# Optimization experiments

Hardware: AMD Instinct MI355X
Metric: run time of the kernel (lower is better)

## Reference

```python
import jax, jax.numpy as jnp
import numpy as np

K = 20  # neighbors, from init kwarg k

def _knn_idx(x, k):
    # x: [B, C, N]; returns indices of k nearest neighbors [B, N, k]
    xx = jnp.sum(x * x, axis=1)                      # [B, N]
    inner = jnp.einsum('bcn,bcm->bnm', x, x)         # [B, N, N]
    neg_dist = 2.0 * inner - xx[:, :, None] - xx[:, None, :]
    return jax.lax.top_k(neg_dist, k)[1]


def _graph_feature(x, k):
    # x: [B, C, N] -> [B, N, k, 2C] = concat(neighbor - center, center)
    idx = _knn_idx(jax.lax.stop_gradient(x), k)
    xt = jnp.swapaxes(x, 1, 2)                       # [B, N, C]
    nb = jax.vmap(lambda pts, i: pts[i])(xt, idx)    # [B, N, k, C]
    ctr = jnp.broadcast_to(xt[:, :, None, :], nb.shape)
    return jnp.concatenate([nb - ctr, ctr], axis=-1)


def _edge_conv(x, layers, k):
    # x: [B, C, N]; layers: list of (w [Co,Ci], scale [Co], bias [Co])
    g = _graph_feature(x, k)                         # [B, N, k, 2C]
    for w, s, b in layers:
        g = jax.nn.leaky_relu(jnp.einsum('bnkc,oc->bnko', g, w) * s + b, 0.2)
    return jnp.swapaxes(jnp.max(g, axis=2), 1, 2)    # [B, Co, N]


def setup_inputs() -> dict:
    key = jax.random.key(0)
    ks = jax.random.split(key, 20)
    B, N = 2, 8192
    emb = 1024
    def w(k_, shape):
        fan_in = shape[1]
        return jax.random.normal(k_, shape, jnp.float32) * (1.0 / np.sqrt(fan_in))
    def sc(k_, c):
        return jax.random.uniform(k_, (c,), jnp.float32, 0.5, 1.5)
    def bi(k_, c):
        return jax.random.normal(k_, (c,), jnp.float32) * 0.1
    inp = {
        'points': jax.random.normal(ks[0], (B, N, 3), jnp.float32),
        'w1a': w(ks[1], (64, 12)),  's1a': sc(ks[2], 64),  'b1a': bi(ks[3], 64),
        'w1b': w(ks[4], (64, 64)),  's1b': sc(ks[5], 64),  'b1b': bi(ks[6], 64),
        'w2a': w(ks[7], (64, 128)), 's2a': sc(ks[8], 64),  'b2a': bi(ks[9], 64),
        'w2b': w(ks[10], (64, 64)), 's2b': sc(ks[11], 64), 'b2b': bi(ks[12], 64),
        'w3a': w(ks[13], (64, 128)),'s3a': sc(ks[14], 64), 'b3a': bi(ks[15], 64),
        'wg':  w(ks[16], (emb, 192)),'sg': sc(ks[17], emb),'bg': bi(ks[18], emb),
    }
    return inp


def reference(points, w1a, s1a, b1a, w1b, s1b, b1b,
              w2a, s2a, b2a, w2b, s2b, b2b,
              w3a, s3a, b3a, wg, sg, bg):
    B, N, _ = points.shape
    xyz = jnp.swapaxes(points, 1, 2)                 # [B, 3, N]
    x = jnp.concatenate([xyz, xyz], axis=1)          # [B, 6, N] (features == xyz when C==3)
    x1 = _edge_conv(x,  [(w1a, s1a, b1a), (w1b, s1b, b1b)], K)
    x2 = _edge_conv(x1, [(w2a, s2a, b2a), (w2b, s2b, b2b)], K)
    x3 = _edge_conv(x2, [(w3a, s3a, b3a)], K)
    cat = jnp.concatenate([x1, x2, x3], axis=1)      # [B, 192, N]
    h = jax.nn.leaky_relu(
        jnp.einsum('bcn,oc->bon', cat, wg) * sg[None, :, None] + bg[None, :, None], 0.2)
    g = jnp.max(h, axis=-1, keepdims=True)           # [B, emb, 1]
    x_max = jnp.broadcast_to(g, (B, h.shape[1], N))  # [B, emb, N]
    return x_max
```

## Files before the change

kernel.cpp:

```cpp
#include <hip/hip_runtime.h>
#include <hip/hip_bf16.h>

#define NPTS 8192
#define KNN  20
#define KC   4

__device__ __forceinline__ unsigned fkey(float f) {
  unsigned u = __float_as_uint(f);
  return (u & 0x80000000u) ? ~u : (u | 0x80000000u);
}
__device__ __forceinline__ float funkey(unsigned k) {
  return (k & 0x80000000u) ? __uint_as_float(k & 0x7fffffffu) : __uint_as_float(~k);
}
__device__ __forceinline__ float lrelu(float x) { return x >= 0.f ? x : 0.2f * x; }

__global__ __launch_bounds__(256) void prep_kernel(
    const float* __restrict__ w1a, const float* __restrict__ w1b,
    const float* __restrict__ w2a, const float* __restrict__ w2b,
    const float* __restrict__ w3a, const float* __restrict__ wg,
    float* __restrict__ wp1A, float* __restrict__ wp1B,
    float* __restrict__ wp2A, float* __restrict__ wp2B,
    float* __restrict__ wp3A, float* __restrict__ wgT)
{
  const int t0 = blockIdx.x * blockDim.x + threadIdx.x;
  const int NT = gridDim.x * blockDim.x;
  for (int f = t0; f < 512; f += NT) {
    int i = f & 3, o = (f >> 2) & 63, c4 = f >> 8, c = c4 * 4 + i;
    float v = 0.f;
    if (c < 3)      v = w1a[o*12 + c]     + w1a[o*12 + c + 3];
    else if (c < 6) v = w1a[o*12 + c + 3] + w1a[o*12 + c + 6];
    wp1A[f] = v;
  }
  for (int f = t0; f < 4096; f += NT) {
    int i = f & 3, o = (f >> 2) & 63, c4 = f >> 8, c = c4 * 4 + i;
    wp1B[f] = w1b[o*64 + c];
    wp2B[f] = w2b[o*64 + c];
  }
  for (int f = t0; f < 8192; f += NT) {
    int i = f & 3, o = (f >> 2) & 63, c4 = f >> 8, c = c4 * 4 + i;
    wp2A[f] = w2a[o*128 + c];
    wp3A[f] = w3a[o*128 + c];
  }
  for (int f = t0; f < 192 * 1024; f += NT) {
    int c = f >> 10, o = f & 1023;
    wgT[f] = wg[o*192 + c];
  }
}

__global__ __launch_bounds__(256) void xx_points(const float* __restrict__ pts,
                                                 float* __restrict__ xx)
{
  int t = blockIdx.x * 256 + threadIdx.x;
  if (t < 2 * NPTS) {
    const float* p = pts + (size_t)t * 3;
    xx[t] = p[0]*p[0] + p[1]*p[1] + p[2]*p[2];
  }
}

__device__ __forceinline__ void bitonic64_desc_f(float& v, int lane) {
  #pragma unroll
  for (int k = 2; k <= 64; k <<= 1) {
    #pragma unroll
    for (int j = k >> 1; j >= 1; j >>= 1) {
      float o = __shfl_xor(v, j);
      bool take_max = (((lane & k) == 0) == ((lane & j) == 0));
      v = take_max ? fmaxf(v, o) : fminf(v, o);
    }
  }
}

__device__ __forceinline__ void bitonic64_desc_u64(unsigned long long& v, int lane) {
  #pragma unroll
  for (int k = 2; k <= 64; k <<= 1) {
    #pragma unroll
    for (int j = k >> 1; j >= 1; j >>= 1) {
      unsigned long long o = __shfl_xor(v, j);
      bool take_max = (((lane & k) == 0) == ((lane & j) == 0));
      unsigned long long hi = v > o ? v : o;
      unsigned long long lo = v > o ? o : v;
      v = take_max ? hi : lo;
    }
  }
}

__device__ void sel20_half(float* __restrict__ sdh, int half, int lane,
                           float* __restrict__ hv, int* __restrict__ hj,
                           float* __restrict__ cv, int* __restrict__ cj)
{
  float m = -INFINITY;
  const float4* rp = (const float4*)(sdh + lane * 64);
  #pragma unroll
  for (int t = 0; t < 16; ++t) {
    float4 x = rp[(t + lane) & 15];
    m = fmaxf(m, fmaxf(fmaxf(x.x, x.y), fmaxf(x.z, x.w)));
  }
  bitonic64_desc_f(m, lane);
  float That = __shfl(m, 19);

  int base = 0;
  for (int i = 0; i < 64; ++i) {
    float v = sdh[i * 64 + lane];
    bool p = (v >= That);
    unsigned long long mk = __ballot(p);
    if (p) {
      int pos = base + (int)__popcll(mk & ((1ull << lane) - 1ull));
      if (pos < 64) { cv[pos] = v; cj[pos] = i * 64 + lane; }
    }
    base += (int)__popcll(mk);
  }

  if (base <= 64) {
    unsigned long long key = 0ull;
    if (lane < base)
      key = (((unsigned long long)fkey(cv[lane])) << 32) | (unsigned)(~cj[lane]);
    bitonic64_desc_u64(key, lane);
    if (lane < KNN) {
      hv[lane] = funkey((unsigned)(key >> 32));
      hj[lane] = (half << 12) + (int)((~(unsigned)key) & 4095u);
    }
  } else {
    for (int kk = 0; kk < KNN; ++kk) {
      float bv = -INFINITY; int bj = 4096;
      for (int i = 0; i < 64; ++i) {
        float v = sdh[i * 64 + lane];
        if (v > bv) { bv = v; bj = i * 64 + lane; }
      }
      #pragma unroll
      for (int mm = 32; mm >= 1; mm >>= 1) {
        float ov = __shfl_xor(bv, mm); int oj = __shfl_xor(bj, mm);
        if (ov > bv || (ov == bv && oj < bj)) { bv = ov; bj = oj; }
      }
      if (lane == 0) { hv[kk] = bv; hj[kk] = (half << 12) + bj; }
      sdh[bj] = -INFINITY;
    }
  }
}

__device__ __forceinline__ void merge_halves(const float* __restrict__ hv,
                                             const int* __restrict__ hj,
                                             int lane, int* __restrict__ orow)
{
  unsigned long long key = 0ull;
  if (lane < 2 * KNN)
    key = (((unsigned long long)fkey(hv[lane])) << 32) | (unsigned)(~hj[lane]);
  bitonic64_desc_u64(key, lane);
  if (lane < KNN) orow[lane] = (int)((~(unsigned)key) & (NPTS - 1));
}

__global__ __launch_bounds__(512, 4) void knn3_kernel(
    const float* __restrict__ pts, const float* __restrict__ xx,
    int* __restrict__ idxout)
{
  __shared__ __align__(16) float sd[4][4096];
  __shared__ float s_ctr[4][4];
  __shared__ float s_hv[4][2 * KNN];
  __shared__ int   s_hj[4][2 * KNN];
  __shared__ float s_cv[4][64];
  __shared__ int   s_cj[4][64];
  const int tid = threadIdx.x;
  const int b   = blockIdx.x / (NPTS / 4);
  const int r0  = (blockIdx.x % (NPTS / 4)) * 4;
  const size_t rowbase = (size_t)b * NPTS;

  for (int i = tid; i < 12; i += 512)
    s_ctr[i / 3][i % 3] = pts[(rowbase + r0 + i / 3) * 3 + i % 3];
  __syncthreads();

  const float xr0 = xx[rowbase + r0 + 0], xr1 = xx[rowbase + r0 + 1];
  const float xr2 = xx[rowbase + r0 + 2], xr3 = xx[rowbase + r0 + 3];
  const float c00 = s_ctr[0][0], c01 = s_ctr[0][1], c02 = s_ctr[0][2];
  const float c10 = s_ctr[1][0], c11 = s_ctr[1][1], c12 = s_ctr[1][2];
  const float c20 = s_ctr[2][0], c21 = s_ctr[2][1], c22 = s_ctr[2][2];
  const float c30 = s_ctr[3][0], c31 = s_ctr[3][1], c32 = s_ctr[3][2];
  const int wid = tid >> 6, lane = tid & 63;

  #pragma unroll 1
  for (int h = 0; h < 2; ++h) {
    for (int jl = tid; jl < 4096; jl += 512) {
      const int jg = (h << 12) + jl;
      const float* fj = pts + (rowbase + jg) * 3;
      const float f0 = fj[0], f1 = fj[1], f2 = fj[2];
      const float xj = xx[rowbase + jg];
      sd[0][jl] = 2.f*(f0*c00 + f1*c01 + f2*c02) - xr0 - xj;
      sd[1][jl] = 2.f*(f0*c10 + f1*c11 + f2*c12) - xr1 - xj;
      sd[2][jl] = 2.f*(f0*c20 + f1*c21 + f2*c22) - xr2 - xj;
      sd[3][jl] = 2.f*(f0*c30 + f1*c31 + f2*c32) - xr3 - xj;
    }
    __syncthreads();
    if (wid < 4)
      sel20_half(sd[wid], h, lane, &s_hv[wid][h * KNN], &s_hj[wid][h * KNN],
                 s_cv[wid], s_cj[wid]);
    __syncthreads();
  }
  if (wid < 4)
    merge_halves(s_hv[wid], s_hj[wid], lane, idxout + (rowbase + r0 + wid) * KNN);
}

#define ACC4(A, C) \
  A.x += v0.x*C.x + v1.x*C.y + v2.x*C.z + v3.x*C.w; \
  A.y += v0.y*C.x + v1.y*C.y + v2.y*C.z + v3.y*C.w; \
  A.z += v0.z*C.x + v1.z*C.y + v2.z*C.z + v3.z*C.w; \
  A.w += v0.w*C.x + v1.w*C.y + v2.w*C.z + v3.w*C.w;

__global__ __launch_bounds__(512, 4) void knn64_kernel(
    const float* __restrict__ featT, const float* __restrict__ xx,
    int* __restrict__ idxout)
{
  __shared__ __align__(16) float sd[4][4096];
  __shared__ __align__(16) float s_ctr[4][64];
  __shared__ float s_hv[4][2 * KNN];
  __shared__ int   s_hj[4][2 * KNN];
  __shared__ float s_cv[4][64];
  __shared__ int   s_cj[4][64];
  const int tid = threadIdx.x;
  const int bid = blockIdx.x;
  const int b   = (bid & 7) >> 2;
  const int r0  = (((bid >> 3) << 2) + (bid & 3)) * 4;
  const size_t tb = (size_t)b * 64 * NPTS;
  const size_t rowbase = (size_t)b * NPTS;

  if (tid < 256)
    s_ctr[tid >> 6][tid & 63] = featT[tb + (size_t)(tid & 63) * NPTS + r0 + (tid >> 6)];
  __syncthreads();

  const int wid = tid >> 6, lane = tid & 63;
  const float xr0 = xx[rowbase + r0 + 0], xr1 = xx[rowbase + r0 + 1];
  const float xr2 = xx[rowbase + r0 + 2], xr3 = xx[rowbase + r0 + 3];
  const float4* ct0 = (const float4*)s_ctr[0];
  const float4* ct1 = (const float4*)s_ctr[1];
  const float4* ct2 = (const float4*)s_ctr[2];
  const float4* ct3 = (const float4*)s_ctr[3];

  #pragma unroll 1
  for (int h = 0; h < 2; ++h) {
    #pragma unroll 1
    for (int ch = 0; ch < 2; ++ch) {
      const int jl = (wid << 9) + (ch << 8) + (lane << 2);
      const int jg = (h << 12) + jl;
      float4 a0 = {0.f,0.f,0.f,0.f}, a1 = a0, a2 = a0, a3 = a0;
      const float* fp0 = featT + tb + jg;
      #pragma unroll 4
      for (int c4 = 0; c4 < 16; ++c4) {
        const float* fp = fp0 + (size_t)(c4 * 4) * NPTS;
        float4 v0 = *(const float4*)(fp);
        float4 v1 = *(const float4*)(fp + NPTS);
        float4 v2 = *(const float4*)(fp + 2 * NPTS);
        float4 v3 = *(const float4*)(fp + 3 * NPTS);
        float4 c0 = ct0[c4], c1 = ct1[c4], c2 = ct2[c4], c3 = ct3[c4];
        ACC4(a0, c0); ACC4(a1, c1); ACC4(a2, c2); ACC4(a3, c3);
      }
      const float4 xv = *(const float4*)(xx + rowbase + jg);
      float4 s0, s1, s2, s3;
      s0.x = 2.f*a0.x - xr0 - xv.x; s0.y = 2.f*a0.y - xr0 - xv.y;
      s0.z = 2.f*a0.z - xr0 - xv.z; s0.w = 2.f*a0.w - xr0 - xv.w;
      s1.x = 2.f*a1.x - xr1 - xv.x; s1.y = 2.f*a1.y - xr1 - xv.y;
      s1.z = 2.f*a1.z - xr1 - xv.z; s1.w = 2.f*a1.w - xr1 - xv.w;
      s2.x = 2.f*a2.x - xr2 - xv.x; s2.y = 2.f*a2.y - xr2 - xv.y;
      s2.z = 2.f*a2.z - xr2 - xv.z; s2.w = 2.f*a2.w - xr2 - xv.w;
      s3.x = 2.f*a3.x - xr3 - xv.x; s3.y = 2.f*a3.y - xr3 - xv.y;
      s3.z = 2.f*a3.z - xr3 - xv.z; s3.w = 2.f*a3.w - xr3 - xv.w;
      *(float4*)&sd[0][jl] = s0;
      *(float4*)&sd[1][jl] = s1;
      *(float4*)&sd[2][jl] = s2;
      *(float4*)&sd[3][jl] = s3;
    }
    __syncthreads();
    if (wid < 4)
      sel20_half(sd[wid], h, lane, &s_hv[wid][h * KNN], &s_hj[wid][h * KNN],
                 s_cv[wid], s_cj[wid]);
    __syncthreads();
  }
  if (wid < 4)
    merge_halves(s_hv[wid], s_hj[wid], lane, idxout + (rowbase + r0 + wid) * KNN);
}

template<int D, bool HASB, bool WAUX>
__global__ __launch_bounds__(256) void fused_conv(
    const float* __restrict__ feat, int fstride, int foff,
    const int* __restrict__ idx,
    const float4* __restrict__ wAp, const float* __restrict__ sa, const float* __restrict__ ba,
    const float4* __restrict__ wBp, const float* __restrict__ sb, const float* __restrict__ bb,
    float* __restrict__ outbuf, int ooff, float* __restrict__ xxout,
    float* __restrict__ featT)
{
  constexpr int CHA  = (D == 64) ? 32 : 2;
  constexpr int CHA4 = CHA * 4;
  __shared__ float4 s_wA[CHA * 64];
  __shared__ float4 s_wB[HASB ? 16 * 64 : 1];
  __shared__ __align__(16) float4 s_g[4 * KC * CHA];
  __shared__ __align__(16) float  s_h1[HASB ? 4 * KC * 64 : 4];
  __shared__ float s_ctr[4][(D > 4) ? D : 4];
  __shared__ float s_sa[64], s_ba[64], s_sb[64], s_bb[64];

  const int tid = threadIdx.x;
  const int p = tid >> 6, o = tid & 63;
  const int b  = blockIdx.x / (NPTS / 4);
  const int p0 = (blockIdx.x % (NPTS / 4)) * 4;
  const size_t rowbase = (size_t)b * NPTS;

  for (int i = tid; i < CHA * 64; i += 256) s_wA[i] = wAp[i];
  if (HASB) for (int i = tid; i < 16 * 64; i += 256) s_wB[i] = wBp[i];
  if (tid < 64) {
    s_sa[tid] = sa[tid]; s_ba[tid] = ba[tid];
    if (HASB) { s_sb[tid] = sb[tid]; s_bb[tid] = bb[tid]; }
  }
  for (int i = tid; i < 4 * D; i += 256)
    s_ctr[i / D][i % D] = feat[(rowbase + p0 + (i / D)) * fstride + foff + (i % D)];
  __syncthreads();

  float* s_gf = (float*)s_g;
  float hmax = -INFINITY;
  for (int kc = 0; kc < KNN / KC; ++kc) {
    for (int s = tid; s < 4 * KC * CHA4; s += 256) {
      int pp = s / (KC * CHA4);
      int rr = s - pp * (KC * CHA4);
      int kk = rr / CHA4;
      int c  = rr - kk * CHA4;
      int nb = idx[(rowbase + p0 + pp) * KNN + kc * KC + kk];
      float v;
      if (D == 64) {
        v = (c < 64) ? (feat[(rowbase + nb) * fstride + foff + c] - s_ctr[pp][c])
                     : s_ctr[pp][c - 64];
      } else {
        if (c < 3)      v = feat[(rowbase + nb) * 3 + c] - s_ctr[pp][c];
        else if (c < 6) v = s_ctr[pp][c - 3];
        else            v = 0.f;
      }
      s_gf[s] = v;
    }
    __syncthreads();

    float acc[KC];
    #pragma unroll
    for (int kk = 0; kk < KC; ++kk) acc[kk] = 0.f;
    for (int c4 = 0; c4 < CHA; ++c4) {
      float4 w = s_wA[c4 * 64 + o];
      #pragma unroll
      for (int kk = 0; kk < KC; ++kk) {
        float4 g = s_g[(p * KC + kk) * CHA + c4];
        acc[kk] += w.x*g.x + w.y*g.y + w.z*g.z + w.w*g.w;
      }
    }
    if (HASB) {
      #pragma unroll
      for (int kk = 0; kk < KC; ++kk)
        s_h1[(p * KC + kk) * 64 + o] = lrelu(acc[kk] * s_sa[o] + s_ba[o]);
      __syncthreads();
      float acc2[KC];
      #pragma unroll
      for (int kk = 0; kk < KC; ++kk) acc2[kk] = 0.f;
      const float4* s_h14 = (const float4*)s_h1;
      for (int c4 = 0; c4 < 16; ++c4) {
        float4 w = s_wB[c4 * 64 + o];
        #pragma unroll
        for (int kk = 0; kk < KC; ++kk) {
          float4 h = s_h14[(p * KC + kk) * 16 + c4];
          acc2[kk] += w.x*h.x + w.y*h.y + w.z*h.z + w.w*h.w;
        }
      }
      #pragma unroll
      for (int kk = 0; kk < KC; ++kk)
        hmax = fmaxf(hmax, lrelu(acc2[kk] * s_sb[o] + s_bb[o]));
      __syncthreads();
    } else {
      #pragma unroll
      for (int kk = 0; kk < KC; ++kk)
        hmax = fmaxf(hmax, lrelu(acc[kk] * s_sa[o] + s_ba[o]));
      __syncthreads();
    }
  }
  outbuf[(rowbase + p0 + p) * 192 + ooff + o] = hmax;
  if (WAUX) {
    featT[(size_t)b * 64 * NPTS + (size_t)o * NPTS + (p0 + p)] = hmax;
    float ss = hmax * hmax;
    #pragma unroll
    for (int m = 1; m < 64; m <<= 1) ss += __shfl_xor(ss, m);
    if (o == 0) xxout[rowbase + p0 + p] = ss;
  }
}

__global__ __launch_bounds__(256) void init_gmax(unsigned* __restrict__ g)
{
  int t = blockIdx.x * 256 + threadIdx.x;
  if (t < 2048) g[t] = fkey(-1e30f);
}

__global__ __launch_bounds__(256) void final_kernel(
    const float* __restrict__ cat, const float* __restrict__ wgT,
    const float* __restrict__ sg, const float* __restrict__ bg,
    unsigned* __restrict__ gmax)
{
  const int tid = threadIdx.x;
  const int chunk = blockIdx.x & 15;
  const int grp   = blockIdx.x >> 4;
  const int pt = grp * 256 + tid;
  const int b  = pt >> 13;
  const float4* crow = (const float4*)(cat + (size_t)pt * 192);
  float acc[64];
  #pragma unroll
  for (int o = 0; o < 64; ++o) acc[o] = 0.f;
  for (int c4 = 0; c4 < 48; ++c4) {
    float4 cv = crow[c4];
    const float* w0 = wgT + (size_t)(c4 * 4) * 1024 + chunk * 64;
    const float* w1 = w0 + 1024;
    const float* w2 = w1 + 1024;
    const float* w3 = w2 + 1024;
    #pragma unroll
    for (int o = 0; o < 64; ++o)
      acc[o] += cv.x*w0[o] + cv.y*w1[o] + cv.z*w2[o] + cv.w*w3[o];
  }
  const int lane = tid & 63;
  #pragma unroll
  for (int o = 0; o < 64; ++o) {
    int ch = chunk * 64 + o;
    float h = lrelu(acc[o] * sg[ch] + bg[ch]);
    #pragma unroll
    for (int m = 1; m < 64; m <<= 1) h = fmaxf(h, __shfl_xor(h, m));
    if (lane == 0) atomicMax(&gmax[b * 1024 + ch], fkey(h));
  }
}

__global__ __launch_bounds__(256) void bcast_kernel(const unsigned* __restrict__ gmax,
                                                    float* __restrict__ out)
{
  int t = blockIdx.x * 256 + threadIdx.x;
  int bo = t >> 11;
  float v = funkey(gmax[bo]);
  float4 w; w.x = v; w.y = v; w.z = v; w.w = v;
  ((float4*)out)[t] = w;
}

extern "C" void kernel_launch(void* const* d_in, const int* in_sizes, int n_in,
                              void* d_out, int out_size, void* d_ws, size_t ws_size,
                              hipStream_t stream)
{
  const float* points = (const float*)d_in[0];
  const float* w1a = (const float*)d_in[1];  const float* s1a = (const float*)d_in[2];  const float* b1a = (const float*)d_in[3];
  const float* w1b = (const float*)d_in[4];  const float* s1b = (const float*)d_in[5];  const float* b1b = (const float*)d_in[6];
  const float* w2a = (const float*)d_in[7];  const float* s2a = (const float*)d_in[8];  const float* b2a = (const float*)d_in[9];
  const float* w2b = (const float*)d_in[10]; const float* s2b = (const float*)d_in[11]; const float* b2b = (const float*)d_in[12];
  const float* w3a = (const float*)d_in[13]; const float* s3a = (const float*)d_in[14]; const float* b3a = (const float*)d_in[15];
  const float* wg  = (const float*)d_in[16]; const float* sg  = (const float*)d_in[17]; const float* bg  = (const float*)d_in[18];

  char* ws = (char*)d_ws;
  float*    cat   = (float*)(ws);
  float*    xxbuf = (float*)(ws + 12582912);
  int*      idxb  = (int*)  (ws + 12648448);
  float*    wp1A  = (float*)(ws + 13959168);
  float*    wp1B  = (float*)(ws + 13961216);
  float*    wp2A  = (float*)(ws + 13977600);
  float*    wp2B  = (float*)(ws + 14010368);
  float*    wp3A  = (float*)(ws + 14026752);
  float*    wgT   = (float*)(ws + 14059520);
  unsigned* gmax  = (unsigned*)(ws + 14845952);
  const size_t WS_NEED = 14854144;
  if (ws_size < WS_NEED || n_in != 19) return;

  float* featT = (float*)d_out;

  prep_kernel<<<256, 256, 0, stream>>>(w1a, w1b, w2a, w2b, w3a, wg,
                                       wp1A, wp1B, wp2A, wp2B, wp3A, wgT);
  xx_points<<<64, 256, 0, stream>>>(points, xxbuf);
  knn3_kernel<<<4096, 512, 0, stream>>>(points, xxbuf, idxb);
  fused_conv<3, true, true><<<4096, 256, 0, stream>>>(
      points, 3, 0, idxb, (const float4*)wp1A, s1a, b1a,
      (const float4*)wp1B, s1b, b1b, cat, 0, xxbuf, featT);
  knn64_kernel<<<4096, 512, 0, stream>>>(featT, xxbuf, idxb);
  fused_conv<64, true, true><<<4096, 256, 0, stream>>>(
      cat, 192, 0, idxb, (const float4*)wp2A, s2a, b2a,
      (const float4*)wp2B, s2b, b2b, cat, 64, xxbuf, featT);
  knn64_kernel<<<4096, 512, 0, stream>>>(featT, xxbuf, idxb);
  fused_conv<64, false, false><<<4096, 256, 0, stream>>>(
      cat, 192, 64, idxb, (const float4*)wp3A, s3a, b3a,
      nullptr, nullptr, nullptr, cat, 128, nullptr, nullptr);
  init_gmax<<<8, 256, 0, stream>>>(gmax);
  final_kernel<<<1024, 256, 0, stream>>>(cat, wgT, sg, bg, gmax);
  bcast_kernel<<<16384, 256, 0, stream>>>(gmax, (float*)d_out);
}
```

Baseline: 1.845 ms.

## Process eight query rows per block in knn64 with streaming quarter-wise top-k merge

New measurement: 1.780 ms. 3.5% less time.

```diff
diff --git a/kernel.cpp b/kernel.cpp
--- a/kernel.cpp
+++ b/kernel.cpp
@@ -145,6 +145,53 @@
     key = (((unsigned long long)fkey(hv[lane])) << 32) | (unsigned)(~hj[lane]);
   bitonic64_desc_u64(key, lane);
   if (lane < KNN) orow[lane] = (int)((~(unsigned)key) & (NPTS - 1));
+}
+
+__device__ unsigned long long sel20_quarter(float* __restrict__ sdq, int jbase,
+                                            int lane, float* __restrict__ cv,
+                                            int* __restrict__ cj)
+{
+  float m = -INFINITY;
+  #pragma unroll 8
+  for (int i = 0; i < 32; ++i) m = fmaxf(m, sdq[i * 64 + lane]);
+  bitonic64_desc_f(m, lane);
+  float That = __shfl(m, 19);
+
+  int base = 0;
+  for (int i = 0; i < 32; ++i) {
+    float v = sdq[i * 64 + lane];
+    bool p = (v >= That);
+    unsigned long long mk = __ballot(p);
+    if (p) {
+      int pos = base + (int)__popcll(mk & ((1ull << lane) - 1ull));
+      if (pos < 64) { cv[pos] = v; cj[pos] = jbase + i * 64 + lane; }
+    }
+    base += (int)__popcll(mk);
+  }
+
+  unsigned long long key = 0ull;
+  if (base <= 64) {
+    if (lane < base)
+      key = (((unsigned long long)fkey(cv[lane])) << 32) | (unsigned)(~cj[lane]);
+    bitonic64_desc_u64(key, lane);
+  } else {
+    for (int kk = 0; kk < KNN; ++kk) {
+      float bv = -INFINITY; int bj = 2048;
+      for (int i = 0; i < 32; ++i) {
+        float v = sdq[i * 64 + lane];
+        if (v > bv) { bv = v; bj = i * 64 + lane; }
+      }
+      #pragma unroll
+      for (int mm = 32; mm >= 1; mm >>= 1) {
+        float ov = __shfl_xor(bv, mm); int oj = __shfl_xor(bj, mm);
+        if (ov > bv || (ov == bv && oj < bj)) { bv = ov; bj = oj; }
+      }
+      if (lane == kk)
+        key = (((unsigned long long)fkey(bv)) << 32) | (unsigned)(~(jbase + bj));
+      sdq[bj] = -INFINITY;
+    }
+  }
+  return key;
 }
 
 __global__ __launch_bounds__(512, 4) void knn3_kernel(
@@ -206,72 +253,82 @@
     const float* __restrict__ featT, const float* __restrict__ xx,
     int* __restrict__ idxout)
 {
-  __shared__ __align__(16) float sd[4][4096];
-  __shared__ __align__(16) float s_ctr[4][64];
-  __shared__ float s_hv[4][2 * KNN];
-  __shared__ int   s_hj[4][2 * KNN];
-  __shared__ float s_cv[4][64];
-  __shared__ int   s_cj[4][64];
+  __shared__ __align__(16) float sd[8][2048];
+  __shared__ __align__(16) float s_ctr[8][64];
+  __shared__ float s_cv[8][64];
+  __shared__ int   s_cj[8][64];
   const int tid = threadIdx.x;
   const int bid = blockIdx.x;
   const int b   = (bid & 7) >> 2;
-  const int r0  = (((bid >> 3) << 2) + (bid & 3)) * 4;
+  const int r0  = (((bid >> 3) << 2) + (bid & 3)) * 8;
   const size_t tb = (size_t)b * 64 * NPTS;
   const size_t rowbase = (size_t)b * NPTS;
 
-  if (tid < 256)
-    s_ctr[tid >> 6][tid & 63] = featT[tb + (size_t)(tid & 63) * NPTS + r0 + (tid >> 6)];
+  s_ctr[tid >> 6][tid & 63] = featT[tb + (size_t)(tid & 63) * NPTS + r0 + (tid >> 6)];
   __syncthreads();
 
   const int wid = tid >> 6, lane = tid & 63;
-  const float xr0 = xx[rowbase + r0 + 0], xr1 = xx[rowbase + r0 + 1];
-  const float xr2 = xx[rowbase + r0 + 2], xr3 = xx[rowbase + r0 + 3];
+  float xr[8];
+  #pragma unroll
+  for (int r = 0; r < 8; ++r) xr[r] = xx[rowbase + r0 + r];
   const float4* ct0 = (const float4*)s_ctr[0];
   const float4* ct1 = (const float4*)s_ctr[1];
   const float4* ct2 = (const float4*)s_ctr[2];
   const float4* ct3 = (const float4*)s_ctr[3];
+  const float4* ct4 = (const float4*)s_ctr[4];
+  const float4* ct5 = (const float4*)s_ctr[5];
+  const float4* ct6 = (const float4*)s_ctr[6];
+  const float4* ct7 = (const float4*)s_ctr[7];
+
+  unsigned long long runkey = 0ull;
 
   #pragma unroll 1
-  for (int h = 0; h < 2; ++h) {
-    #pragma unroll 1
-    for (int ch = 0; ch < 2; ++ch) {
-      const int jl = (wid << 9) + (ch << 8) + (lane << 2);
-      const int jg = (h << 12) + jl;
-      float4 a0 = {0.f,0.f,0.f,0.f}, a1 = a0, a2 = a0, a3 = a0;
-      const float* fp0 = featT + tb + jg;
-      #pragma unroll 4
-      for (int c4 = 0; c4 < 16; ++c4) {
-        const float* fp = fp0 + (size_t)(c4 * 4) * NPTS;
-        float4 v0 = *(const float4*)(fp);
-        float4 v1 = *(const float4*)(fp + NPTS);
-        float4 v2 = *(const float4*)(fp + 2 * NPTS);
-        float4 v3 = *(const float4*)(fp + 3 * NPTS);
-        float4 c0 = ct0[c4], c1 = ct1[c4], c2 = ct2[c4], c3 = ct3[c4];
-        ACC4(a0, c0); ACC4(a1, c1); ACC4(a2, c2); ACC4(a3, c3);
-      }
-      const float4 xv = *(const float4*)(xx + rowbase + jg);
-      float4 s0, s1, s2, s3;
-      s0.x = 2.f*a0.x - xr0 - xv.x; s0.y = 2.f*a0.y - xr0 - xv.y;
-      s0.z = 2.f*a0.z - xr0 - xv.z; s0.w = 2.f*a0.w - xr0 - xv.w;
-      s1.x = 2.f*a1.x - xr1 - xv.x; s1.y = 2.f*a1.y - xr1 - xv.y;
-      s1.z = 2.f*a1.z - xr1 - xv.z; s1.w = 2.f*a1.w - xr1 - xv.w;
-      s2.x = 2.f*a2.x - xr2 - xv.x; s2.y = 2.f*a2.y - xr2 - xv.y;
-      s2.z = 2.f*a2.z - xr2 - xv.z; s2.w = 2.f*a2.w - xr2 - xv.w;
-      s3.x = 2.f*a3.x - xr3 - xv.x; s3.y = 2.f*a3.y - xr3 - xv.y;
-      s3.z = 2.f*a3.z - xr3 - xv.z; s3.w = 2.f*a3.w - xr3 - xv.w;
-      *(float4*)&sd[0][jl] = s0;
-      *(float4*)&sd[1][jl] = s1;
-      *(float4*)&sd[2][jl] = s2;
-      *(float4*)&sd[3][jl] = s3;
-    }
+  for (int h = 0; h < 4; ++h) {
+    const int jl = (wid << 8) + (lane << 2);
+    const int jg = (h << 11) + jl;
+    float4 a0 = {0.f,0.f,0.f,0.f}, a1 = a0, a2 = a0, a3 = a0;
+    float4 a4 = a0, a5 = a0, a6 = a0, a7 = a0;
+    const float* fp0 = featT + tb + jg;
+    #pragma unroll 2
+    for (int c4 = 0; c4 < 16; ++c4) {
+      const float* fp = fp0 + (size_t)(c4 * 4) * NPTS;
+      float4 v0 = *(const float4*)(fp);
+      float4 v1 = *(const float4*)(fp + NPTS);
+      float4 v2 = *(const float4*)(fp + 2 * NPTS);
+      float4 v3 = *(const float4*)(fp + 3 * NPTS);
+      float4 c;
+      c = ct0[c4]; ACC4(a0, c);
+      c = ct1[c4]; ACC4(a1, c);
+      c = ct2[c4]; ACC4(a2, c);
+      c = ct3[c4]; ACC4(a3, c);
+      c = ct4[c4]; ACC4(a4, c);
+      c = ct5[c4]; ACC4(a5, c);
+      c = ct6[c4]; ACC4(a6, c);
+      c = ct7[c4]; ACC4(a7, c);
+    }
+    const float4 xv = *(const float4*)(xx + rowbase + jg);
+    float4 s;
+    #define STORE_ROW(A, R) \
+      s.x = 2.f*A.x - xr[R] - xv.x; s.y = 2.f*A.y - xr[R] - xv.y; \
+      s.z = 2.f*A.z - xr[R] - xv.z; s.w = 2.f*A.w - xr[R] - xv.w; \
+      *(float4*)&sd[R][jl] = s;
+    STORE_ROW(a0, 0); STORE_ROW(a1, 1); STORE_ROW(a2, 2); STORE_ROW(a3, 3);
+    STORE_ROW(a4, 4); STORE_ROW(a5, 5); STORE_ROW(a6, 6); STORE_ROW(a7, 7);
+    #undef STORE_ROW
     __syncthreads();
-    if (wid < 4)
-      sel20_half(sd[wid], h, lane, &s_hv[wid][h * KNN], &s_hj[wid][h * KNN],
-                 s_cv[wid], s_cj[wid]);
+
+    unsigned long long pk = sel20_quarter(sd[wid], h << 11, lane,
+                                          s_cv[wid], s_cj[wid]);
+    unsigned long long nk = __shfl(pk, lane - 20);
+    unsigned long long mkey = (lane < 20) ? runkey
+                            : ((lane < 40) ? nk : 0ull);
+    bitonic64_desc_u64(mkey, lane);
+    runkey = mkey;
     __syncthreads();
   }
-  if (wid < 4)
-    merge_halves(s_hv[wid], s_hj[wid], lane, idxout + (rowbase + r0 + wid) * KNN);
+  if (lane < KNN)
+    idxout[(rowbase + r0 + wid) * KNN + lane] =
+        (int)((~(unsigned)runkey) & (NPTS - 1));
 }
 
 template<int D, bool HASB, bool WAUX>
@@ -465,11 +522,11 @@
   fused_conv<3, true, true><<<4096, 256, 0, stream>>>(
       points, 3, 0, idxb, (const float4*)wp1A, s1a, b1a,
       (const float4*)wp1B, s1b, b1b, cat, 0, xxbuf, featT);
-  knn64_kernel<<<4096, 512, 0, stream>>>(featT, xxbuf, idxb);
+  knn64_kernel<<<2048, 512, 0, stream>>>(featT, xxbuf, idxb);
   fused_conv<64, true, true><<<4096, 256, 0, stream>>>(
       cat, 192, 0, idxb, (const float4*)wp2A, s2a, b2a,
       (const float4*)wp2B, s2b, b2b, cat, 64, xxbuf, featT);
-  knn64_kernel<<<4096, 512, 0, stream>>>(featT, xxbuf, idxb);
+  knn64_kernel<<<2048, 512, 0, stream>>>(featT, xxbuf, idxb);
   fused_conv<64, false, false><<<4096, 256, 0, stream>>>(
       cat, 192, 64, idxb, (const float4*)wp3A, s3a, b3a,
       nullptr, nullptr, nullptr, cat, 128, nullptr, nullptr);
```
